# Performance work log

Hardware: AMD Instinct MI355X
Metric: run time of the kernel (lower is better)

Reference implementation:

```python
import jax, jax.numpy as jnp
import numpy as np

N_NODES = 50000
N_EDGES = 600000
D_IN = 128
D_OUT = 128


def setup_inputs() -> dict:
    key = jax.random.key(0)
    k1, k2, k3, k4, k5, k6 = jax.random.split(key, 6)
    n_feats = jax.random.normal(k1, (N_NODES, D_IN), dtype=jnp.float32)
    e_weights = jax.random.uniform(k2, (N_EDGES, 1), dtype=jnp.float32)
    # Linear(in_dim*2, out_dim): W [out, 2*in], b [out]
    W = jax.random.normal(k3, (D_OUT, 2 * D_IN), dtype=jnp.float32) * 0.05
    b = jax.random.normal(k4, (D_OUT,), dtype=jnp.float32) * 0.05
    src = jax.random.randint(k5, (N_EDGES,), 0, N_NODES, dtype=jnp.int64)
    dst = jax.random.randint(k6, (N_EDGES,), 0, N_NODES, dtype=jnp.int64)
    return {"n_feats": n_feats, "e_weights": e_weights, "W": W, "b": b,
            "src": src, "dst": dst}


def reference(n_feats, e_weights, W, b, src, dst):
    N = n_feats.shape[0]
    # message: u_mul_e -> h[src] * ew   [E, D]
    msgs = n_feats[src] * e_weights
    # mean reduce over incoming edges (DGL fn.mean divides by in-degree)
    agg = jax.ops.segment_sum(msgs, dst, num_segments=N)  # [N, D]
    deg = jax.ops.segment_sum(jnp.ones((msgs.shape[0],), dtype=n_feats.dtype),
                              dst, num_segments=N)         # [N]
    h = agg / jnp.maximum(deg, 1.0)[:, None]               # zero-degree -> 0
    # concat aggregated + original, then linear
    z = jnp.concatenate([h, n_feats], axis=-1)             # [N, 2D]
    return z @ W.T + b
```

## Files before the change

### kernel.cpp

```cpp
#include <hip/hip_runtime.h>

#define N_NODES 50000
#define N_EDGES 600000
#define DIM 128
#define WGN (256 * 128 / 8)
#define GEMM_PAIRS ((N_NODES + 63) / 64)
#define K2_BLOCKS (GEMM_PAIRS * 3)
#define ZERO_BLOCKS ((N_NODES + 255) / 256)
#define BCAP 64
#define EPH 1024

typedef __attribute__((ext_vector_type(8))) short short8;
typedef __attribute__((ext_vector_type(4))) float f32x4;

__device__ __forceinline__ unsigned bf16rne(float f) {
  unsigned x = __float_as_uint(f);
  x += 0x7fffu + ((x >> 16) & 1u);
  return x >> 16;
}

__device__ __forceinline__ uint2 pack4(float4 v) {
  uint2 o;
  o.x = bf16rne(v.x) | (bf16rne(v.y) << 16);
  o.y = bf16rne(v.z) | (bf16rne(v.w) << 16);
  return o;
}

__device__ __forceinline__ void fma8(float* a, uint4 v, float w) {
  a[0] += __uint_as_float(v.x << 16) * w;
  a[1] += __uint_as_float(v.x & 0xffff0000u) * w;
  a[2] += __uint_as_float(v.y << 16) * w;
  a[3] += __uint_as_float(v.y & 0xffff0000u) * w;
  a[4] += __uint_as_float(v.z << 16) * w;
  a[5] += __uint_as_float(v.z & 0xffff0000u) * w;
  a[6] += __uint_as_float(v.w << 16) * w;
  a[7] += __uint_as_float(v.w & 0xffff0000u) * w;
}

__global__ __launch_bounds__(256) void k_zero_wts(
    int* __restrict__ deg, const float* __restrict__ Wf,
    uint4* __restrict__ wtS) {
  int gid = blockIdx.x * 256 + threadIdx.x;
  if (gid < N_NODES) deg[gid] = 0;
  if (gid < WGN) {
    int j = gid >> 4, cb = gid & 15;
    int jr = (j < 128) ? j : (j - 128);
    int c0 = ((j < 128) ? 0 : 128) + cb * 8;
    const float4* s = reinterpret_cast<const float4*>(Wf + (size_t)jr * 256 + c0);
    uint2 lo = pack4(s[0]);
    uint2 hi = pack4(s[1]);
    int jb = j >> 4, l16 = j & 15, ks = cb >> 2, lg = cb & 3;
    wtS[((jb * 4 + ks) * 64) + lg * 16 + l16] = make_uint4(lo.x, lo.y, hi.x, hi.y);
  }
}

__global__ __launch_bounds__(256) void k_gemm_histscat(
    const int* __restrict__ dst, const int* __restrict__ src,
    const float* __restrict__ ew, int* __restrict__ deg,
    unsigned* __restrict__ srcw,
    const float* __restrict__ nf, const uint4* __restrict__ wtS,
    const float* __restrict__ bias,
    unsigned short* __restrict__ y1, unsigned short* __restrict__ y2) {
  __shared__ char As[16384];
  const int grp = blockIdx.x / 3;
  const int sub = blockIdx.x % 3;

  if (sub == 2) {
    const int e0 = grp * EPH + threadIdx.x;
    int d[4];
    unsigned rec[4];
    bool v[4];
#pragma unroll
    for (int k = 0; k < 4; ++k) {
      int e = e0 + k * 256;
      v[k] = (e < N_EDGES);
      d[k] = 0; rec[k] = 0;
      if (v[k]) {
        d[k] = dst[e];
        unsigned wq = (unsigned)rintf(ew[e] * 65535.0f);
        rec[k] = (unsigned)src[e] | (wq << 16);
      }
    }
    int rk[4];
#pragma unroll
    for (int k = 0; k < 4; ++k)
      if (v[k]) rk[k] = atomicAdd(&deg[d[k]], 1);
#pragma unroll
    for (int k = 0; k < 4; ++k)
      if (v[k]) srcw[d[k] * BCAP + rk[k]] = rec[k];
    return;
  }

  const int node0 = grp * 64;
  const int jsel = sub;
  const int tid = threadIdx.x;

#pragma unroll
  for (int i = 0; i < 8; ++i) {
    int G = tid + i * 256;
    int r = G >> 5, c = G & 31;
    int node = node0 + r;
    if (node > N_NODES - 1) node = N_NODES - 1;
    float4 v = *reinterpret_cast<const float4*>(nf + (size_t)node * DIM + c * 4);
    uint2 p = pack4(v);
    int g = c >> 1, half = c & 1;
    *reinterpret_cast<uint2*>(As + r * 256 + ((g ^ (r & 7)) * 16) + half * 8) = p;
  }
  __syncthreads();

  const int lane = tid & 63;
  const int wv = tid >> 6;
  const int l16 = lane & 15, lg = lane >> 4;

  f32x4 acc[4][2] = {};
#pragma unroll
  for (int ks = 0; ks < 4; ++ks) {
    short8 anf[4], awt[2];
#pragma unroll
    for (int m = 0; m < 4; ++m) {
      int r = m * 16 + l16;
      int g = ks * 4 + lg;
      anf[m] = *reinterpret_cast<const short8*>(As + r * 256 + ((g ^ (r & 7)) * 16));
    }
#pragma unroll
    for (int n = 0; n < 2; ++n) {
      int jb = jsel * 8 + wv * 2 + n;
      const uint4* fp = wtS + (jb * 4 + ks) * 64 + lane;
      uint4 v = *fp;
      awt[n] = *reinterpret_cast<const short8*>(&v);
    }
#pragma unroll
    for (int m = 0; m < 4; ++m)
#pragma unroll
      for (int n = 0; n < 2; ++n)
        acc[m][n] = __builtin_amdgcn_mfma_f32_16x16x32_bf16(awt[n], anf[m], acc[m][n], 0, 0, 0);
  }

  unsigned short* yb = jsel ? y2 : y1;
#pragma unroll
  for (int n = 0; n < 2; ++n) {
    int jb = (wv * 2 + n) * 16 + lg * 4;
    float4 bv = make_float4(0.f, 0.f, 0.f, 0.f);
    if (jsel) bv = *reinterpret_cast<const float4*>(bias + jb);
#pragma unroll
    for (int m = 0; m < 4; ++m) {
      int node = node0 + m * 16 + l16;
      if (node >= N_NODES) continue;
      uint2 st;
      st.x = bf16rne(acc[m][n][0] + bv.x) | (bf16rne(acc[m][n][1] + bv.y) << 16);
      st.y = bf16rne(acc[m][n][2] + bv.z) | (bf16rne(acc[m][n][3] + bv.w) << 16);
      *reinterpret_cast<uint2*>(yb + (size_t)node * 128 + jb) = st;
    }
  }
}

__global__ __launch_bounds__(256) void k_gather(
    const uint4* __restrict__ y1q,
    const uint4* __restrict__ y2q,
    const int* __restrict__ deg, const unsigned* __restrict__ srcw,
    float4* __restrict__ out4) {
  int node = blockIdx.x * 4 + (threadIdx.x >> 6);
  int lane = threadIdx.x & 63;
  int g = lane >> 3;
  int c = lane & 7;
  int dg = deg[node];
  const unsigned* bucket = srcw + (size_t)node * BCAP;

  float a[16];
#pragma unroll
  for (int k = 0; k < 16; ++k) a[k] = 0.f;

  for (int j = g; j < dg; j += 8) {
    unsigned q = bucket[j];
    float w = (float)(q >> 16) * (1.0f / 65535.0f);
    const uint4* rp = y1q + (size_t)(q & 0xffffu) * 16 + c * 2;
    uint4 v0 = rp[0];
    uint4 v1 = rp[1];
    fma8(a, v0, w);
    fma8(a + 8, v1, w);
  }
#pragma unroll
  for (int k = 0; k < 16; ++k) {
    a[k] += __shfl_xor(a[k], 8);
    a[k] += __shfl_xor(a[k], 16);
    a[k] += __shfl_xor(a[k], 32);
  }
  if (g == 0) {
    float inv = 1.0f / (float)max(dg, 1);
    uint4 u0 = y2q[(size_t)node * 16 + c * 2];
    uint4 u1 = y2q[(size_t)node * 16 + c * 2 + 1];
    float4 o0, o1, o2, o3;
    o0.x = a[0] * inv + __uint_as_float(u0.x << 16);
    o0.y = a[1] * inv + __uint_as_float(u0.x & 0xffff0000u);
    o0.z = a[2] * inv + __uint_as_float(u0.y << 16);
    o0.w = a[3] * inv + __uint_as_float(u0.y & 0xffff0000u);
    o1.x = a[4] * inv + __uint_as_float(u0.z << 16);
    o1.y = a[5] * inv + __uint_as_float(u0.z & 0xffff0000u);
    o1.z = a[6] * inv + __uint_as_float(u0.w << 16);
    o1.w = a[7] * inv + __uint_as_float(u0.w & 0xffff0000u);
    o2.x = a[8] * inv + __uint_as_float(u1.x << 16);
    o2.y = a[9] * inv + __uint_as_float(u1.x & 0xffff0000u);
    o2.z = a[10] * inv + __uint_as_float(u1.y << 16);
    o2.w = a[11] * inv + __uint_as_float(u1.y & 0xffff0000u);
    o3.x = a[12] * inv + __uint_as_float(u1.z << 16);
    o3.y = a[13] * inv + __uint_as_float(u1.z & 0xffff0000u);
    o3.z = a[14] * inv + __uint_as_float(u1.w << 16);
    o3.w = a[15] * inv + __uint_as_float(u1.w & 0xffff0000u);
    float4* op = out4 + (size_t)node * 32 + c * 4;
    op[0] = o0; op[1] = o1; op[2] = o2; op[3] = o3;
  }
}

extern "C" void kernel_launch(void* const* d_in, const int* in_sizes, int n_in,
                              void* d_out, int out_size, void* d_ws, size_t ws_size,
                              hipStream_t stream) {
  const float* nf  = (const float*)d_in[0];
  const float* ew  = (const float*)d_in[1];
  const float* W   = (const float*)d_in[2];
  const float* b   = (const float*)d_in[3];
  const int*   src = (const int*)d_in[4];
  const int*   dst = (const int*)d_in[5];
  float* out = (float*)d_out;

  char* ws = (char*)d_ws;
  char* wtS  = ws;
  char* y1   = wtS + (size_t)WGN * 16;
  char* y2   = y1 + (size_t)N_NODES * DIM * 2;
  unsigned* srcw = (unsigned*)(y2 + (size_t)N_NODES * DIM * 2);
  int*  deg  = (int*)(srcw + (size_t)N_NODES * BCAP);

  k_zero_wts<<<ZERO_BLOCKS, 256, 0, stream>>>(deg, W, (uint4*)wtS);
  k_gemm_histscat<<<K2_BLOCKS, 256, 0, stream>>>(
      dst, src, ew, deg, srcw, nf, (const uint4*)wtS, b,
      (unsigned short*)y1, (unsigned short*)y2);
  k_gather<<<N_NODES / 4, 256, 0, stream>>>(
      (const uint4*)y1, (const uint4*)y2, deg, srcw, (float4*)out);
}
```

Before: 78.12 us.

## Two-pass binned edge scatter to localize degree atomics and bucket writes

The direct per-edge atomic scatter into node buckets is replaced by two passes. First, edges are partitioned into coarse destination bins using shared-memory counters and a staging buffer. Then a separate kernel processes each bin and performs the degree atomics and bucket writes inside a localized address range. This aims to cut scattered global atomics and improve cache locality. In exchange it adds a kernel launch, extra staging traffic, and only 98 blocks for the second pass, and it risks overflow if a bin exceeds its fixed capacity.

```diff
diff --git a/kernel.cpp b/kernel.cpp
--- a/kernel.cpp
+++ b/kernel.cpp
@@ -5,10 +5,12 @@
 #define DIM 128
 #define WGN (256 * 128 / 8)
 #define GEMM_PAIRS ((N_NODES + 63) / 64)
-#define K2_BLOCKS (GEMM_PAIRS * 3)
+#define K1_BLOCKS (GEMM_PAIRS * 3)
 #define ZERO_BLOCKS ((N_NODES + 255) / 256)
 #define BCAP 64
-#define EPH 1024
+#define BINS 98
+#define BINCAP 8192
+#define P1_BLOCKS ((N_EDGES + 1023) / 1024)
 
 typedef __attribute__((ext_vector_type(8))) short short8;
 typedef __attribute__((ext_vector_type(4))) float f32x4;
@@ -38,10 +40,11 @@
 }
 
 __global__ __launch_bounds__(256) void k_zero_wts(
-    int* __restrict__ deg, const float* __restrict__ Wf,
-    uint4* __restrict__ wtS) {
+    int* __restrict__ deg, int* __restrict__ gcnt,
+    const float* __restrict__ Wf, uint4* __restrict__ wtS) {
   int gid = blockIdx.x * 256 + threadIdx.x;
   if (gid < N_NODES) deg[gid] = 0;
+  if (gid < BINS) gcnt[gid] = 0;
   if (gid < WGN) {
     int j = gid >> 4, cb = gid & 15;
     int jr = (j < 128) ? j : (j - 128);
@@ -54,46 +57,57 @@
   }
 }
 
-__global__ __launch_bounds__(256) void k_gemm_histscat(
+__global__ __launch_bounds__(256) void k_gemm_p1(
     const int* __restrict__ dst, const int* __restrict__ src,
-    const float* __restrict__ ew, int* __restrict__ deg,
-    unsigned* __restrict__ srcw,
+    const float* __restrict__ ew, int* __restrict__ gcnt,
+    uint2* __restrict__ binbuf,
     const float* __restrict__ nf, const uint4* __restrict__ wtS,
     const float* __restrict__ bias,
     unsigned short* __restrict__ y1, unsigned short* __restrict__ y2) {
   __shared__ char As[16384];
   const int grp = blockIdx.x / 3;
   const int sub = blockIdx.x % 3;
+  const int tid = threadIdx.x;
 
   if (sub == 2) {
-    const int e0 = grp * EPH + threadIdx.x;
-    int d[4];
-    unsigned rec[4];
-    bool v[4];
+    if (grp >= P1_BLOCKS) return;
+    int* lcnt = reinterpret_cast<int*>(As);
+    int* lbase = reinterpret_cast<int*>(As + 512);
+    if (tid < BINS) lcnt[tid] = 0;
+    __syncthreads();
+
+    const int e0 = grp * 1024 + tid;
+    int d4[4], r4[4];
+    unsigned rec4[4];
+    bool v4[4];
 #pragma unroll
     for (int k = 0; k < 4; ++k) {
       int e = e0 + k * 256;
-      v[k] = (e < N_EDGES);
-      d[k] = 0; rec[k] = 0;
-      if (v[k]) {
-        d[k] = dst[e];
+      v4[k] = (e < N_EDGES);
+      d4[k] = 0; rec4[k] = 0; r4[k] = 0;
+      if (v4[k]) {
+        d4[k] = dst[e];
         unsigned wq = (unsigned)rintf(ew[e] * 65535.0f);
-        rec[k] = (unsigned)src[e] | (wq << 16);
+        rec4[k] = (unsigned)src[e] | (wq << 16);
+        r4[k] = atomicAdd(&lcnt[d4[k] >> 9], 1);
       }
     }
-    int rk[4];
-#pragma unroll
-    for (int k = 0; k < 4; ++k)
-      if (v[k]) rk[k] = atomicAdd(&deg[d[k]], 1);
-#pragma unroll
-    for (int k = 0; k < 4; ++k)
-      if (v[k]) srcw[d[k] * BCAP + rk[k]] = rec[k];
+    __syncthreads();
+    if (tid < BINS) lbase[tid] = atomicAdd(&gcnt[tid], lcnt[tid]);
+    __syncthreads();
+#pragma unroll
+    for (int k = 0; k < 4; ++k) {
+      if (v4[k]) {
+        int bin = d4[k] >> 9;
+        binbuf[(size_t)bin * BINCAP + lbase[bin] + r4[k]] =
+            make_uint2(rec4[k], (unsigned)d4[k]);
+      }
+    }
     return;
   }
 
   const int node0 = grp * 64;
   const int jsel = sub;
-  const int tid = threadIdx.x;
 
 #pragma unroll
   for (int i = 0; i < 8; ++i) {
@@ -154,9 +168,22 @@
   }
 }
 
+__global__ __launch_bounds__(256) void k_p2(
+    const int* __restrict__ gcnt, const uint2* __restrict__ binbuf,
+    int* __restrict__ deg, unsigned* __restrict__ srcw) {
+  const int b = blockIdx.x;
+  const int n = gcnt[b];
+  const uint2* bb = binbuf + (size_t)b * BINCAP;
+  for (int i = threadIdx.x; i < n; i += 256) {
+    uint2 rec = bb[i];
+    int d = (int)rec.y;
+    int rk = atomicAdd(&deg[d], 1);
+    srcw[d * BCAP + rk] = rec.x;
+  }
+}
+
 __global__ __launch_bounds__(256) void k_gather(
-    const uint4* __restrict__ y1q,
-    const uint4* __restrict__ y2q,
+    const uint4* __restrict__ y1q, const uint4* __restrict__ y2q,
     const int* __restrict__ deg, const unsigned* __restrict__ srcw,
     float4* __restrict__ out4) {
   int node = blockIdx.x * 4 + (threadIdx.x >> 6);
@@ -227,12 +254,15 @@
   char* y1   = wtS + (size_t)WGN * 16;
   char* y2   = y1 + (size_t)N_NODES * DIM * 2;
   unsigned* srcw = (unsigned*)(y2 + (size_t)N_NODES * DIM * 2);
-  int*  deg  = (int*)(srcw + (size_t)N_NODES * BCAP);
-
-  k_zero_wts<<<ZERO_BLOCKS, 256, 0, stream>>>(deg, W, (uint4*)wtS);
-  k_gemm_histscat<<<K2_BLOCKS, 256, 0, stream>>>(
-      dst, src, ew, deg, srcw, nf, (const uint4*)wtS, b,
+  int* deg   = (int*)(srcw + (size_t)N_NODES * BCAP);
+  int* gcnt  = deg + N_NODES;
+  uint2* binbuf = (uint2*)((char*)(gcnt + 128));
+
+  k_zero_wts<<<ZERO_BLOCKS, 256, 0, stream>>>(deg, gcnt, W, (uint4*)wtS);
+  k_gemm_p1<<<K1_BLOCKS, 256, 0, stream>>>(
+      dst, src, ew, gcnt, binbuf, nf, (const uint4*)wtS, b,
       (unsigned short*)y1, (unsigned short*)y2);
+  k_p2<<<BINS, 256, 0, stream>>>(gcnt, binbuf, deg, srcw);
   k_gather<<<N_NODES / 4, 256, 0, stream>>>(
       (const uint4*)y1, (const uint4*)y2, deg, srcw, (float4*)out);
 }
```

Measured after the change: 88.42 us. +13.2%, slower.
